# Performance work log

Hardware: AMD Instinct MI355X
Metric: run time of the kernel (lower is better)

The kernel has to match this reference:

```python
import jax, jax.numpy as jnp
import numpy as np

# ---- box encoding helpers ----

def _cv2_corners(b):
    # b: [..., 5] (cx, cy, w, h, angle) -> [..., 4, 2] rotated-rect vertices
    cx, cy, w, h, a = (b[..., i] for i in range(5))
    c, s = jnp.cos(a), jnp.sin(a)
    dx, dy = w * 0.5, h * 0.5
    lx = jnp.stack([-dx, dx, dx, -dx], axis=-1)   # [..., 4]
    ly = jnp.stack([-dy, -dy, dy, dy], axis=-1)
    x = cx[..., None] + lx * c[..., None] - ly * s[..., None]
    y = cy[..., None] + lx * s[..., None] + ly * c[..., None]
    return jnp.stack([x, y], axis=-1)


def _vertices_to_cv2(v):
    # v: [..., 4, 2] ordered vertices -> [..., 5] (cx, cy, w, h, angle)
    ctr = v.mean(axis=-2)
    e1 = v[..., 1, :] - v[..., 0, :]
    e2 = v[..., 3, :] - v[..., 0, :]
    w = jnp.linalg.norm(e1, axis=-1)
    h = jnp.linalg.norm(e2, axis=-1)
    ang = jnp.arctan2(e1[..., 1], e1[..., 0])
    return jnp.concatenate([ctr, w[..., None], h[..., None], ang[..., None]], axis=-1)


def _corners_to_hbb(corners):
    # [..., 4, 2] -> [..., 4] (x1, y1, x2, y2)
    return jnp.concatenate([corners.min(axis=-2), corners.max(axis=-2)], axis=-1)


def _box_iou(a, b):
    # a: [B, N, 4], b: [B, M, 4] -> [B, N, M] axis-aligned IoU
    lt = jnp.maximum(a[:, :, None, :2], b[:, None, :, :2])
    rb = jnp.minimum(a[:, :, None, 2:], b[:, None, :, 2:])
    wh = jnp.clip(rb - lt, 0.0)
    inter = wh[..., 0] * wh[..., 1]
    area_a = (a[..., 2] - a[..., 0]) * (a[..., 3] - a[..., 1])
    area_b = (b[..., 2] - b[..., 0]) * (b[..., 3] - b[..., 1])
    union = area_a[:, :, None] + area_b[:, None, :] - inter
    return inter / jnp.clip(union, 1e-7)


def setup_inputs() -> dict:
    key = jax.random.key(0)
    ks = jax.random.split(key, 6)
    B, N, M, C = 8, 16384, 128, 81

    def rand_boxes(k, shape):
        k1, k2, k3 = jax.random.split(k, 3)
        ctr = jax.random.uniform(k1, shape + (2,), minval=0.0, maxval=1000.0)
        wh = jax.random.uniform(k2, shape + (2,), minval=16.0, maxval=160.0)
        ang = jax.random.uniform(k3, shape + (1,), minval=-1.5, maxval=1.5)
        return jnp.concatenate([ctr, wh, ang], axis=-1)

    box_pred = rand_boxes(ks[0], (B, N))
    gt = rand_boxes(ks[1], (B, M))
    # seed the first M predictions near the GT so positives (IoU>=0.5) exist
    box_pred = box_pred.at[:, :M].set(gt + 2.0 * jax.random.normal(ks[2], gt.shape))
    regression_targets = _cv2_corners(gt)                     # [B, M, 4, 2] vertices
    classification_targets = jax.random.randint(ks[3], (B, M), 0, C - 1)
    class_pred = jax.random.normal(ks[4], (B, N, C))
    return {
        "box_pred": box_pred,
        "class_pred": class_pred,
        "regression_targets": regression_targets,
        "classification_targets": classification_targets,
        "n_samples": 256,
    }


def reference(box_pred, class_pred, regression_targets, classification_targets, n_samples):
    B = box_pred.shape[0]
    C = class_pred.shape[-1]
    background_cls = C - 1
    k_pos = n_samples // 2
    k_neg = n_samples - k_pos

    box_targets_cv2 = _vertices_to_cv2(regression_targets)           # [B, M, 5]
    hbb_pred = _corners_to_hbb(_cv2_corners(box_pred))               # [B, N, 4]
    hbb_tgt = _corners_to_hbb(regression_targets)                    # [B, M, 4]
    iou = _box_iou(hbb_pred, hbb_tgt)                                # [B, N, M]

    def per_image(iou_i, labels_i, logits_i, boxp_i, boxt_i):
        max_iou = iou_i.max(axis=-1)                                 # [N]
        match = iou_i.argmax(axis=-1)                                # [N] matched GT idx
        pos_mask = max_iou >= 0.5
        # sample up to k_pos positives (highest IoU) and k_neg negatives (lowest IoU)
        pos_score = jnp.where(pos_mask, max_iou, -1.0)
        _, pos_idx = jax.lax.top_k(pos_score, k_pos)
        pos_valid = pos_mask[pos_idx]
        neg_score = jnp.where(pos_mask, -jnp.inf, -max_iou)
        _, neg_idx = jax.lax.top_k(neg_score, k_neg)
        neg_valid = ~pos_mask[neg_idx]
        # classification targets: matched GT label for positives, background otherwise
        cls_target = jnp.where(pos_mask, labels_i[match], background_cls)
        sel_idx = jnp.concatenate([pos_idx, neg_idx])                # [n_samples]
        sel_valid = jnp.concatenate([pos_valid, neg_valid])
        logp = jax.nn.log_softmax(logits_i[sel_idx], axis=-1)        # [n_samples, C]
        nll = -jnp.take_along_axis(logp, cls_target[sel_idx][:, None], axis=1)[:, 0]
        cls_loss = jnp.sum(nll * sel_valid.astype(logp.dtype))
        rel_pred = boxp_i[pos_idx]                                   # [k_pos, 5]
        rel_gt = boxt_i[match[pos_idx]]                              # [k_pos, 5]
        d = jnp.abs(rel_pred - rel_gt)
        sl1 = jnp.where(d < 1.0, 0.5 * d * d, d - 0.5)
        regr_loss = jnp.sum(sl1 * pos_valid[:, None].astype(sl1.dtype))
        return cls_loss, regr_loss

    cls_l, reg_l = jax.vmap(per_image)(
        iou, classification_targets, class_pred, box_pred, box_targets_cv2
    )
    classification_loss = cls_l.sum() / B
    regression_loss = reg_l.sum() / B
    total_loss = classification_loss + regression_loss
    return total_loss, classification_loss, regression_loss
```

## Files before the change

kernel.cpp:

```cpp
#include <hip/hip_runtime.h>
#include <math.h>

#define B_ 8
#define N_ 16384
#define M_ 128
#define C_ 81
#define TPB 512
#define KPT 32
#define NWAVE (TPB / 64)

__global__ __launch_bounds__(256)
void iou_fused(const float* __restrict__ bp,
               const float* __restrict__ rt,
               float* __restrict__ miou,
               int* __restrict__ match,
               float* __restrict__ out) {
    __shared__ float sx1[M_], sy1[M_], sx2[M_], sy2[M_], sab[M_];
    int b = blockIdx.y;
    int n = blockIdx.x * blockDim.x + threadIdx.x;

    if (blockIdx.x == 0 && blockIdx.y == 0 && threadIdx.x < 3)
        out[threadIdx.x] = 0.0f;

    if (threadIdx.x < M_) {
        const float* v = rt + ((size_t)b * M_ + threadIdx.x) * 8;
        float x0 = v[0], y0 = v[1], x1 = v[2], y1 = v[3];
        float x2 = v[4], y2 = v[5], x3 = v[6], y3 = v[7];
        float mnx = fminf(fminf(x0, x1), fminf(x2, x3));
        float mny = fminf(fminf(y0, y1), fminf(y2, y3));
        float mxx = fmaxf(fmaxf(x0, x1), fmaxf(x2, x3));
        float mxy = fmaxf(fmaxf(y0, y1), fmaxf(y2, y3));
        sx1[threadIdx.x] = mnx; sy1[threadIdx.x] = mny;
        sx2[threadIdx.x] = mxx; sy2[threadIdx.x] = mxy;
        sab[threadIdx.x] = (mxx - mnx) * (mxy - mny);
    }
    __syncthreads();

    const float* p = bp + ((size_t)b * N_ + n) * 5;
    float cx = p[0], cy = p[1], w = p[2], h = p[3], a = p[4];
    float c = cosf(a), s = sinf(a);
    float dx = w * 0.5f, dy = h * 0.5f;
    float ex = fabsf(dx * c) + fabsf(dy * s);
    float ey = fabsf(dx * s) + fabsf(dy * c);
    float ax1 = cx - ex, ay1 = cy - ey, ax2 = cx + ex, ay2 = cy + ey;
    float area_a = (ax2 - ax1) * (ay2 - ay1);

    float bin = -1.0f, bun = 1.0f;
    int bm = 0;
#pragma unroll 4
    for (int m = 0; m < M_; m++) {
        float lx = fmaxf(ax1, sx1[m]), ly = fmaxf(ay1, sy1[m]);
        float rx = fminf(ax2, sx2[m]), ry = fminf(ay2, sy2[m]);
        float ww = fmaxf(rx - lx, 0.0f), hh = fmaxf(ry - ly, 0.0f);
        float inter = ww * hh;
        float uni = fmaxf(area_a + sab[m] - inter, 1e-7f);
        bool better = inter * bun > bin * uni;
        bin = better ? inter : bin;
        bun = better ? uni : bun;
        bm = better ? m : bm;
    }
    miou[(size_t)b * N_ + n] = bin / bun;
    match[(size_t)b * N_ + n] = bm;
}

__device__ __forceinline__ unsigned wave_sum6(unsigned c) {
    unsigned s = 0;
#pragma unroll
    for (int bit = 0; bit < 6; bit++)
        s += (unsigned)__popcll(__ballot((c >> bit) & 1u)) << bit;
    return s;
}

__device__ __forceinline__ unsigned bsum(unsigned c, unsigned* slot) {
    unsigned ws = wave_sum6(c);
    if ((threadIdx.x & 63) == 0) slot[threadIdx.x >> 6] = ws;
    __syncthreads();
    unsigned r = 0;
#pragma unroll
    for (int i = 0; i < NWAVE; i++) r += slot[i];
    return r;
}

__global__ __launch_bounds__(TPB)
void select_loss(const float* __restrict__ miou, const int* __restrict__ match,
                 const float* __restrict__ logits, const float* __restrict__ bp,
                 const float* __restrict__ rt, const int* __restrict__ labels,
                 const int* __restrict__ ns_ptr, float* __restrict__ out) {
    int type = blockIdx.x;
    int b = blockIdx.y;
    __shared__ float s_cv2[5][M_];
    __shared__ unsigned red[2 * NWAVE] __attribute__((aligned(16)));
    __shared__ float fredc[NWAVE], fredr[NWAVE];
    __shared__ unsigned sel[256];
    __shared__ unsigned selcnt;

    int tid = threadIdx.x;
    int lane = tid & 63, wv = tid >> 6;
    if (tid == 0) selcnt = 0;

    if (tid < M_) {
        const float* v = rt + ((size_t)b * M_ + tid) * 8;
        float x0 = v[0], y0 = v[1], x1 = v[2], y1 = v[3];
        float x2 = v[4], y2 = v[5], x3 = v[6], y3 = v[7];
        s_cv2[0][tid] = (x0 + x1 + x2 + x3) * 0.25f;
        s_cv2[1][tid] = (y0 + y1 + y2 + y3) * 0.25f;
        float e1x = x1 - x0, e1y = y1 - y0;
        float e2x = x3 - x0, e2y = y3 - y0;
        s_cv2[2][tid] = sqrtf(e1x * e1x + e1y * e1y);
        s_cv2[3][tid] = sqrtf(e2x * e2x + e2y * e2y);
        s_cv2[4][tid] = atan2f(e1y, e1x);
    }

    int ns = ns_ptr[0];
    unsigned ktar = (type == 0) ? (unsigned)(ns / 2) : (unsigned)(ns - ns / 2);
    if (ktar > 256u) ktar = 256u;

    const float4* mi4 = (const float4*)(miou + (size_t)b * N_);
    int base = tid * KPT;
    unsigned key[KPT];
    unsigned vcnt = 0;
#pragma unroll
    for (int q = 0; q < KPT / 4; q++) {
        float4 v4 = mi4[tid * (KPT / 4) + q];
        float io[4] = {v4.x, v4.y, v4.z, v4.w};
#pragma unroll
        for (int j = 0; j < 4; j++) {
            bool pos = (io[j] >= 0.5f);
            unsigned k;
            if (type == 0) {
                if (pos) { k = ~(__float_as_uint(io[j]) | 0x80000000u); vcnt++; }
                else k = 0xFFFFFFFFu;
            } else {
                if (!pos) { k = __float_as_uint(io[j]) | 0x80000000u; vcnt++; }
                else k = 0xFFFFFFFFu;
            }
            key[q * 4 + j] = k;
        }
    }
    __syncthreads();

    int pc = 0;
    unsigned V = bsum(vcnt, red + NWAVE * ((pc++) & 1));
    unsigned keff = (ktar < V) ? ktar : V;

    if (keff == V) {
#pragma unroll
        for (int j = 0; j < KPT; j++) {
            if (key[j] != 0xFFFFFFFFu) {
                unsigned p = atomicAdd(&selcnt, 1u);
                sel[p] = (unsigned)(base + j);
            }
        }
    } else {
        unsigned Ckey;
        bool found = false;
        if (type == 1) {
            unsigned cmin = 0;
#pragma unroll
            for (int j = 0; j < KPT; j++) cmin += (key[j] <= 0x80000000u) ? 1u : 0u;
            unsigned tot = bsum(cmin, red + NWAVE * ((pc++) & 1));
            if (tot >= keff) { Ckey = 0x80000000u; found = true; }
        }
        if (!found) {
            unsigned lo = 0, hi = 0xFFFFFFFFu;
            while (lo < hi) {
                unsigned mid = lo + ((hi - lo) >> 1);
                unsigned c = 0;
#pragma unroll
                for (int j = 0; j < KPT; j++) c += (key[j] <= mid) ? 1u : 0u;
                unsigned tot = bsum(c, red + NWAVE * ((pc++) & 1));
                if (tot >= keff) hi = mid; else lo = mid + 1;
            }
            Ckey = lo;
        }

        unsigned cl = 0, ce = 0;
#pragma unroll
        for (int j = 0; j < KPT; j++) {
            cl += (key[j] < Ckey) ? 1u : 0u;
            ce += (key[j] == Ckey) ? 1u : 0u;
        }
        unsigned m = bsum(cl, red + NWAVE * ((pc++) & 1));
        unsigned e = keff - m;

        unsigned sc = ce;
#pragma unroll
        for (int o = 1; o < 64; o <<= 1) {
            unsigned t = __shfl_up(sc, o);
            if (lane >= o) sc += t;
        }
        unsigned* slot = red + NWAVE * ((pc++) & 1);
        if (lane == 63) slot[wv] = sc;
        __syncthreads();
        unsigned off = 0;
        for (int i = 0; i < wv; i++) off += slot[i];
        unsigned rank = off + sc - ce;

#pragma unroll
        for (int j = 0; j < KPT; j++) {
            unsigned k = key[j];
            bool s = false;
            if (k < Ckey) s = true;
            else if (k == Ckey) { s = (rank < e); rank++; }
            if (s) {
                unsigned p = atomicAdd(&selcnt, 1u);
                sel[p] = (unsigned)(base + j);
            }
        }
    }
    __syncthreads();
    unsigned total_sel = selcnt;

    float cls_sum = 0.f, reg_sum = 0.f;
    int q = tid & 3;
    for (unsigned sm = (unsigned)(tid >> 2); sm < total_sel; sm += TPB / 4) {
        unsigned i = sel[sm];
        const float* row = logits + ((size_t)b * N_ + i) * C_;
        int c0 = q * 21;
        int c1 = (c0 + 21 < C_) ? c0 + 21 : C_;
        float mx = -INFINITY;
        for (int c = c0; c < c1; c++) mx = fmaxf(mx, row[c]);
        mx = fmaxf(mx, __shfl_xor(mx, 1));
        mx = fmaxf(mx, __shfl_xor(mx, 2));
        float se = 0.f;
        for (int c = c0; c < c1; c++) se += expf(row[c] - mx);
        se += __shfl_xor(se, 1);
        se += __shfl_xor(se, 2);
        if (q == 0) {
            float lse = mx + logf(se);
            if (type == 0) {
                int g_gt = match[(size_t)b * N_ + i];
                int tc = labels[b * M_ + g_gt];
                cls_sum += lse - row[tc];
                const float* pp = bp + ((size_t)b * N_ + i) * 5;
#pragma unroll
                for (int d = 0; d < 5; d++) {
                    float ad = fabsf(pp[d] - s_cv2[d][g_gt]);
                    reg_sum += (ad < 1.f) ? 0.5f * ad * ad : ad - 0.5f;
                }
            } else {
                cls_sum += lse - row[C_ - 1];
            }
        }
    }

#pragma unroll
    for (int o = 32; o; o >>= 1) {
        cls_sum += __shfl_down(cls_sum, o);
        reg_sum += __shfl_down(reg_sum, o);
    }
    if (lane == 0) { fredc[wv] = cls_sum; fredr[wv] = reg_sum; }
    __syncthreads();
    if (tid == 0) {
        float cs = 0.f, rs = 0.f;
#pragma unroll
        for (int i = 0; i < NWAVE; i++) { cs += fredc[i]; rs += fredr[i]; }
        const float invB = 1.0f / (float)B_;
        atomicAdd(&out[0], (cs + rs) * invB);
        atomicAdd(&out[1], cs * invB);
        atomicAdd(&out[2], rs * invB);
    }
}

extern "C" void kernel_launch(void* const* d_in, const int* in_sizes, int n_in,
                              void* d_out, int out_size, void* d_ws, size_t ws_size,
                              hipStream_t stream) {
    const float* box_pred = (const float*)d_in[0];
    const float* class_pred = (const float*)d_in[1];
    const float* reg_tgt = (const float*)d_in[2];
    const int* cls_tgt = (const int*)d_in[3];
    const int* n_samples = (const int*)d_in[4];

    float* ws = (float*)d_ws;
    float* miou = ws;
    int* match = (int*)(miou + (size_t)B_ * N_);
    float* out = (float*)d_out;

    iou_fused<<<dim3(N_ / 256, B_), 256, 0, stream>>>(box_pred, reg_tgt, miou, match, out);
    select_loss<<<dim3(2, B_), TPB, 0, stream>>>(miou, match, class_pred, box_pred,
                                                 reg_tgt, cls_tgt, n_samples, out);
}
```

Measured before the change: 130.4 us.

## Two-level per-wave top-k selection and register-blocked IoU with packed float4 boxes

```diff
diff --git a/kernel.cpp b/kernel.cpp
--- a/kernel.cpp
+++ b/kernel.cpp
@@ -15,64 +15,92 @@
                float* __restrict__ miou,
                int* __restrict__ match,
                float* __restrict__ out) {
-    __shared__ float sx1[M_], sy1[M_], sx2[M_], sy2[M_], sab[M_];
+    __shared__ float4 sbox[M_];
     int b = blockIdx.y;
-    int n = blockIdx.x * blockDim.x + threadIdx.x;
-
-    if (blockIdx.x == 0 && blockIdx.y == 0 && threadIdx.x < 3)
-        out[threadIdx.x] = 0.0f;
-
-    if (threadIdx.x < M_) {
-        const float* v = rt + ((size_t)b * M_ + threadIdx.x) * 8;
+    int tid = threadIdx.x;
+
+    if (blockIdx.x == 0 && b == 0 && tid < 3) out[tid] = 0.0f;
+
+    if (tid < M_) {
+        const float* v = rt + ((size_t)b * M_ + tid) * 8;
         float x0 = v[0], y0 = v[1], x1 = v[2], y1 = v[3];
         float x2 = v[4], y2 = v[5], x3 = v[6], y3 = v[7];
         float mnx = fminf(fminf(x0, x1), fminf(x2, x3));
         float mny = fminf(fminf(y0, y1), fminf(y2, y3));
         float mxx = fmaxf(fmaxf(x0, x1), fmaxf(x2, x3));
         float mxy = fmaxf(fmaxf(y0, y1), fmaxf(y2, y3));
-        sx1[threadIdx.x] = mnx; sy1[threadIdx.x] = mny;
-        sx2[threadIdx.x] = mxx; sy2[threadIdx.x] = mxy;
-        sab[threadIdx.x] = (mxx - mnx) * (mxy - mny);
-    }
-    __syncthreads();
-
-    const float* p = bp + ((size_t)b * N_ + n) * 5;
-    float cx = p[0], cy = p[1], w = p[2], h = p[3], a = p[4];
-    float c = cosf(a), s = sinf(a);
-    float dx = w * 0.5f, dy = h * 0.5f;
-    float ex = fabsf(dx * c) + fabsf(dy * s);
-    float ey = fabsf(dx * s) + fabsf(dy * c);
-    float ax1 = cx - ex, ay1 = cy - ey, ax2 = cx + ex, ay2 = cy + ey;
-    float area_a = (ax2 - ax1) * (ay2 - ay1);
-
-    float bin = -1.0f, bun = 1.0f;
-    int bm = 0;
-#pragma unroll 4
+        sbox[tid] = make_float4(mnx, mny, mxx, mxy);
+    }
+    __syncthreads();
+
+    int p0 = blockIdx.x * 512 + tid;
+    float ax1[2], ay1[2], ax2[2], ay2[2], aa[2];
+#pragma unroll
+    for (int t = 0; t < 2; t++) {
+        const float* p = bp + ((size_t)b * N_ + p0 + 256 * t) * 5;
+        float cx = p[0], cy = p[1], w = p[2], h = p[3], a = p[4];
+        float c = cosf(a), s = sinf(a);
+        float dx = w * 0.5f, dy = h * 0.5f;
+        float ex = fabsf(dx * c) + fabsf(dy * s);
+        float ey = fabsf(dx * s) + fabsf(dy * c);
+        ax1[t] = cx - ex; ay1[t] = cy - ey; ax2[t] = cx + ex; ay2[t] = cy + ey;
+        aa[t] = (ax2[t] - ax1[t]) * (ay2[t] - ay1[t]);
+    }
+    float bin[2] = {-1.f, -1.f}, bun[2] = {1.f, 1.f};
+    int bm[2] = {0, 0};
+#pragma unroll 2
     for (int m = 0; m < M_; m++) {
-        float lx = fmaxf(ax1, sx1[m]), ly = fmaxf(ay1, sy1[m]);
-        float rx = fminf(ax2, sx2[m]), ry = fminf(ay2, sy2[m]);
-        float ww = fmaxf(rx - lx, 0.0f), hh = fmaxf(ry - ly, 0.0f);
-        float inter = ww * hh;
-        float uni = fmaxf(area_a + sab[m] - inter, 1e-7f);
-        bool better = inter * bun > bin * uni;
-        bin = better ? inter : bin;
-        bun = better ? uni : bun;
-        bm = better ? m : bm;
-    }
-    miou[(size_t)b * N_ + n] = bin / bun;
-    match[(size_t)b * N_ + n] = bm;
-}
-
-__device__ __forceinline__ unsigned wave_sum6(unsigned c) {
+        float4 bb = sbox[m];
+        float ab = (bb.z - bb.x) * (bb.w - bb.y);
+#pragma unroll
+        for (int t = 0; t < 2; t++) {
+            float lx = fmaxf(ax1[t], bb.x), ly = fmaxf(ay1[t], bb.y);
+            float rx = fminf(ax2[t], bb.z), ry = fminf(ay2[t], bb.w);
+            float ww = fmaxf(rx - lx, 0.0f), hh = fmaxf(ry - ly, 0.0f);
+            float inter = ww * hh;
+            float uni = fmaxf(aa[t] + ab - inter, 1e-7f);
+            bool better = inter * bun[t] > bin[t] * uni;
+            bin[t] = better ? inter : bin[t];
+            bun[t] = better ? uni : bun[t];
+            bm[t] = better ? m : bm[t];
+        }
+    }
+#pragma unroll
+    for (int t = 0; t < 2; t++) {
+        miou[(size_t)b * N_ + p0 + 256 * t] = bin[t] / bun[t];
+        match[(size_t)b * N_ + p0 + 256 * t] = bm[t];
+    }
+}
+
+__device__ __forceinline__ unsigned wsum6(unsigned c) {
     unsigned s = 0;
 #pragma unroll
     for (int bit = 0; bit < 6; bit++)
         s += (unsigned)__popcll(__ballot((c >> bit) & 1u)) << bit;
     return s;
 }
-
-__device__ __forceinline__ unsigned bsum(unsigned c, unsigned* slot) {
-    unsigned ws = wave_sum6(c);
+__device__ __forceinline__ unsigned wprefix6(unsigned c, unsigned long long lt) {
+    unsigned s = 0;
+#pragma unroll
+    for (int bit = 0; bit < 6; bit++)
+        s += (unsigned)__popcll(__ballot((c >> bit) & 1u) & lt) << bit;
+    return s;
+}
+__device__ __forceinline__ unsigned wsum2(unsigned c) {
+    return (unsigned)__popcll(__ballot(c & 1u)) +
+           ((unsigned)__popcll(__ballot((c >> 1) & 1u)) << 1);
+}
+__device__ __forceinline__ unsigned bsum6(unsigned c, unsigned* slot) {
+    unsigned ws = wsum6(c);
+    if ((threadIdx.x & 63) == 0) slot[threadIdx.x >> 6] = ws;
+    __syncthreads();
+    unsigned r = 0;
+#pragma unroll
+    for (int i = 0; i < NWAVE; i++) r += slot[i];
+    return r;
+}
+__device__ __forceinline__ unsigned bsum2(unsigned c, unsigned* slot) {
+    unsigned ws = wsum2(c);
     if ((threadIdx.x & 63) == 0) slot[threadIdx.x >> 6] = ws;
     __syncthreads();
     unsigned r = 0;
@@ -91,11 +119,14 @@
     __shared__ float s_cv2[5][M_];
     __shared__ unsigned red[2 * NWAVE] __attribute__((aligned(16)));
     __shared__ float fredc[NWAVE], fredr[NWAVE];
+    __shared__ unsigned cand_key[NWAVE * 128];
+    __shared__ unsigned cand_idx[NWAVE * 128];
     __shared__ unsigned sel[256];
     __shared__ unsigned selcnt;
 
     int tid = threadIdx.x;
     int lane = tid & 63, wv = tid >> 6;
+    unsigned long long ltmask = ((unsigned long long)1 << lane) - 1ull;
     if (tid == 0) selcnt = 0;
 
     if (tid < M_) {
@@ -140,7 +171,7 @@
     __syncthreads();
 
     int pc = 0;
-    unsigned V = bsum(vcnt, red + NWAVE * ((pc++) & 1));
+    unsigned V = bsum6(vcnt, red + NWAVE * ((pc++) & 1));
     unsigned keff = (ktar < V) ? ktar : V;
 
     if (keff == V) {
@@ -152,60 +183,91 @@
             }
         }
     } else {
-        unsigned Ckey;
-        bool found = false;
-        if (type == 1) {
-            unsigned cmin = 0;
-#pragma unroll
-            for (int j = 0; j < KPT; j++) cmin += (key[j] <= 0x80000000u) ? 1u : 0u;
-            unsigned tot = bsum(cmin, red + NWAVE * ((pc++) & 1));
-            if (tot >= keff) { Ckey = 0x80000000u; found = true; }
-        }
-        if (!found) {
-            unsigned lo = 0, hi = 0xFFFFFFFFu;
+        unsigned Vw = wsum6(vcnt);
+        unsigned kw = (Vw < 128u) ? Vw : 128u;
+        unsigned wbase = wv * 128u;
+        if (kw > 0) {
+            unsigned lo = (type == 0) ? 0x40000000u : 0x80000000u;
+            unsigned hi = (type == 0) ? 0x41000000u : 0xBF000000u;
+            if (type == 1) {
+                unsigned c = 0;
+#pragma unroll
+                for (int j = 0; j < KPT; j++) c += (key[j] <= 0x80000000u) ? 1u : 0u;
+                if (wsum6(c) >= kw) { lo = hi = 0x80000000u; }
+            }
             while (lo < hi) {
                 unsigned mid = lo + ((hi - lo) >> 1);
                 unsigned c = 0;
 #pragma unroll
                 for (int j = 0; j < KPT; j++) c += (key[j] <= mid) ? 1u : 0u;
-                unsigned tot = bsum(c, red + NWAVE * ((pc++) & 1));
-                if (tot >= keff) hi = mid; else lo = mid + 1;
-            }
-            Ckey = lo;
-        }
-
-        unsigned cl = 0, ce = 0;
-#pragma unroll
-        for (int j = 0; j < KPT; j++) {
-            cl += (key[j] < Ckey) ? 1u : 0u;
-            ce += (key[j] == Ckey) ? 1u : 0u;
-        }
-        unsigned m = bsum(cl, red + NWAVE * ((pc++) & 1));
+                if (wsum6(c) >= kw) hi = mid; else lo = mid + 1;
+            }
+            unsigned cutW = lo;
+            unsigned clw = 0, cew = 0;
+#pragma unroll
+            for (int j = 0; j < KPT; j++) {
+                clw += (key[j] < cutW) ? 1u : 0u;
+                cew += (key[j] == cutW) ? 1u : 0u;
+            }
+            unsigned mw = wsum6(clw);
+            unsigned ew = kw - mw;
+            unsigned r = wprefix6(cew, ltmask);
+            unsigned selc = 0;
+            unsigned selMask = 0;
+#pragma unroll
+            for (int j = 0; j < KPT; j++) {
+                bool tie = (key[j] == cutW);
+                bool s = (key[j] < cutW) || (tie && r < ew);
+                if (tie) r++;
+                if (s) { selMask |= (1u << j); selc++; }
+            }
+            unsigned woff = wprefix6(selc, ltmask);
+#pragma unroll
+            for (int j = 0; j < KPT; j++) {
+                if ((selMask >> j) & 1u) {
+                    cand_key[wbase + woff] = key[j];
+                    cand_idx[wbase + woff] = (unsigned)(base + j);
+                    woff++;
+                }
+            }
+        }
+        for (unsigned p = kw + (unsigned)lane; p < 128u; p += 64u) {
+            cand_key[wbase + p] = 0xFFFFFFFFu;
+            cand_idx[wbase + p] = 0u;
+        }
+        __syncthreads();
+
+        unsigned ck0 = cand_key[tid], ck1 = cand_key[tid + TPB];
+        unsigned ci0 = cand_idx[tid], ci1 = cand_idx[tid + TPB];
+        unsigned lo = (type == 0) ? 0x40000000u : 0x80000000u;
+        unsigned hi = (type == 0) ? 0x41000000u : 0xBF000000u;
+        while (lo < hi) {
+            unsigned mid = lo + ((hi - lo) >> 1);
+            unsigned c = ((ck0 <= mid) ? 1u : 0u) + ((ck1 <= mid) ? 1u : 0u);
+            unsigned tot = bsum2(c, red + NWAVE * ((pc++) & 1));
+            if (tot >= keff) hi = mid; else lo = mid + 1;
+        }
+        unsigned Ckey = lo;
+        unsigned c2 = ((ck0 < Ckey) ? 1u : 0u) + ((ck1 < Ckey) ? 1u : 0u);
+        unsigned m = bsum2(c2, red + NWAVE * ((pc++) & 1));
         unsigned e = keff - m;
-
-        unsigned sc = ce;
-#pragma unroll
-        for (int o = 1; o < 64; o <<= 1) {
-            unsigned t = __shfl_up(sc, o);
-            if (lane >= o) sc += t;
-        }
-        unsigned* slot = red + NWAVE * ((pc++) & 1);
-        if (lane == 63) slot[wv] = sc;
-        __syncthreads();
-        unsigned off = 0;
-        for (int i = 0; i < wv; i++) off += slot[i];
-        unsigned rank = off + sc - ce;
-
-#pragma unroll
-        for (int j = 0; j < KPT; j++) {
-            unsigned k = key[j];
-            bool s = false;
-            if (k < Ckey) s = true;
-            else if (k == Ckey) { s = (rank < e); rank++; }
-            if (s) {
-                unsigned p = atomicAdd(&selcnt, 1u);
-                sel[p] = (unsigned)(base + j);
-            }
+        unsigned X = 0xFFFFFFFFu;
+        if (e > 0) {
+            unsigned ilo = 0, ihi = N_ - 1;
+            while (ilo < ihi) {
+                unsigned mid = ilo + ((ihi - ilo) >> 1);
+                unsigned c = ((ck0 == Ckey && ci0 <= mid) ? 1u : 0u) +
+                             ((ck1 == Ckey && ci1 <= mid) ? 1u : 0u);
+                unsigned tot = bsum2(c, red + NWAVE * ((pc++) & 1));
+                if (tot >= e) ihi = mid; else ilo = mid + 1;
+            }
+            X = ilo;
+        }
+        if ((ck0 < Ckey) || (ck0 == Ckey && e > 0 && ci0 <= X)) {
+            unsigned p = atomicAdd(&selcnt, 1u); sel[p] = ci0;
+        }
+        if ((ck1 < Ckey) || (ck1 == Ckey && e > 0 && ci1 <= X)) {
+            unsigned p = atomicAdd(&selcnt, 1u); sel[p] = ci1;
         }
     }
     __syncthreads();
@@ -276,7 +338,7 @@
     int* match = (int*)(miou + (size_t)B_ * N_);
     float* out = (float*)d_out;
 
-    iou_fused<<<dim3(N_ / 256, B_), 256, 0, stream>>>(box_pred, reg_tgt, miou, match, out);
+    iou_fused<<<dim3(N_ / 512, B_), 256, 0, stream>>>(box_pred, reg_tgt, miou, match, out);
     select_loss<<<dim3(2, B_), TPB, 0, stream>>>(miou, match, class_pred, box_pred,
                                                  reg_tgt, cls_tgt, n_samples, out);
 }
```

After: 135.7 us. +4.1%, slower.
